# Kernel optimization log

Measured on AMD Instinct MI355X. Metric: run time of the kernel, lower is better.

## Reference

```python
import jax, jax.numpy as jnp
import numpy as np
from jax import lax

B, S, I, H, O, T = 8, 1024, 512, 1024, 512, 8
THRESH = 0.5


def setup_inputs() -> dict:
    key = jax.random.key(0)
    k = jax.random.split(key, 5)
    return {
        "x": jax.random.normal(k[0], (B, S, I), dtype=jnp.float32),
        "w1": jax.random.normal(k[1], (H, I), dtype=jnp.float32) * (1.0 / np.sqrt(I)),
        "b1": jax.random.normal(k[2], (H,), dtype=jnp.float32) * 0.01,
        "w2": jax.random.normal(k[3], (O, H), dtype=jnp.float32) * (1.0 / np.sqrt(H)),
        "b2": jax.random.normal(k[4], (O,), dtype=jnp.float32) * 0.01,
    }


def reference(x, w1, b1, w2, b2):
    # x: (B, S, I). Precompute the input current once (same every timestep).
    inp_cur = jnp.einsum("bsi,hi->bsh", x, w1) + b1  # (B, S, H)
    mem1_0 = jnp.zeros((B, S, H), dtype=x.dtype)
    mem2_0 = jnp.zeros((B, S, O), dtype=x.dtype)

    def step(carry, _):
        mem1, mem2 = carry
        mem1 = mem1 + inp_cur
        spike1 = (mem1 > THRESH).astype(x.dtype)
        mem1 = mem1 * (mem1 <= THRESH).astype(x.dtype)  # reset fired neurons
        mem2 = mem2 + jnp.einsum("bsh,oh->bso", spike1, w2) + b2
        spike2 = (mem2 > THRESH).astype(x.dtype)
        mem2 = mem2 * (mem2 <= THRESH).astype(x.dtype)
        return (mem1, mem2), spike2

    _, spikes = lax.scan(step, (mem1_0, mem2_0), None, length=T)  # (T, B, S, O)
    return jnp.moveaxis(spikes, 0, 1)  # stack on dim=1 -> (B, T, S, O)
```

## Files before the change

### kernel.cpp

```cpp
#include <hip/hip_runtime.h>

static constexpr int B_ = 8, S_ = 1024, I_ = 512, H_ = 1024, O_ = 512, T_ = 8;
static constexpr int M_ = B_ * S_;
static constexpr float TH = 0.5f;

__global__ __launch_bounds__(256) void k1(const float* __restrict__ X,
                                          const float* __restrict__ W1,
                                          const float* __restrict__ B1,
                                          unsigned char* __restrict__ SPB) {
  __shared__ float As[16][132];
  __shared__ float Bs[16][68];
  const int tid = threadIdx.x;
  const int tx = tid & 15, ty = tid >> 4;
  const int rowBase = blockIdx.x * 128, colBase = blockIdx.y * 64;

  float acc[8][4];
#pragma unroll
  for (int i = 0; i < 8; ++i)
#pragma unroll
    for (int j = 0; j < 4; ++j) acc[i][j] = 0.f;

  for (int it = 0; it < 32; ++it) {
#pragma unroll
    for (int l = 0; l < 2; ++l) {
      int f = tid + l * 256;
      int rr = f >> 2, kq = (f & 3) << 2;
      float4 va = *(const float4*)&X[(size_t)(rowBase + rr) * I_ + it * 16 + kq];
      As[kq + 0][rr] = va.x; As[kq + 1][rr] = va.y;
      As[kq + 2][rr] = va.z; As[kq + 3][rr] = va.w;
    }
    {
      int rr = tid >> 2, kq = (tid & 3) << 2;
      float4 vb = *(const float4*)&W1[(size_t)(colBase + rr) * I_ + it * 16 + kq];
      Bs[kq + 0][rr] = vb.x; Bs[kq + 1][rr] = vb.y;
      Bs[kq + 2][rr] = vb.z; Bs[kq + 3][rr] = vb.w;
    }
    __syncthreads();
#pragma unroll
    for (int k = 0; k < 16; ++k) {
      float a[8], b[4];
      *(float4*)&a[0] = *(const float4*)&As[k][ty * 8];
      *(float4*)&a[4] = *(const float4*)&As[k][ty * 8 + 4];
      *(float4*)&b[0] = *(const float4*)&Bs[k][tx * 4];
#pragma unroll
      for (int i = 0; i < 8; ++i)
#pragma unroll
        for (int j = 0; j < 4; ++j) acc[i][j] = fmaf(a[i], b[j], acc[i][j]);
    }
    __syncthreads();
  }

#pragma unroll
  for (int i = 0; i < 8; ++i) {
    int row = rowBase + ty * 8 + i;
    unsigned char by[4];
#pragma unroll
    for (int j = 0; j < 4; ++j) {
      int col = colBase + tx * 4 + j;
      float c = acc[i][j] + B1[col];
      float m = 0.f;
      unsigned bits = 0;
#pragma unroll
      for (int t = 0; t < 8; ++t) {
        m = m + c;
        bool s = m > TH;
        bits |= (s ? 1u : 0u) << t;
        m = s ? 0.f : m;
      }
      by[j] = (unsigned char)bits;
    }
    uchar4 pk; pk.x = by[0]; pk.y = by[1]; pk.z = by[2]; pk.w = by[3];
    *(uchar4*)&SPB[(size_t)row * H_ + colBase + tx * 4] = pk;
  }
}

__global__ __launch_bounds__(256) void k2(const unsigned char* __restrict__ SP,
                                          const float* __restrict__ W2,
                                          const float* __restrict__ B2,
                                          float* __restrict__ out, int t) {
  __shared__ float As0[16][68];
  __shared__ float As1[16][68];
  __shared__ float Bs0[16][68];
  __shared__ float Bs1[16][68];
  const int tid = threadIdx.x;
  const int tx = tid & 15, ty = tid >> 4;
  const int rowBase = blockIdx.x * 64, colBase = blockIdx.y * 64;

  float cur0[4][4], cur1[4][4];
#pragma unroll
  for (int i = 0; i < 4; ++i)
#pragma unroll
    for (int j = 0; j < 4; ++j) { cur0[i][j] = 0.f; cur1[i][j] = 0.f; }

  for (int it = 0; it < 32; ++it) {
    {
      int rr = tid >> 2, bq = (tid & 3) << 2;
      unsigned u0 = *(const unsigned*)&SP[(size_t)(rowBase + rr) * H_ + it * 16 + bq];
      As0[bq + 0][rr] = (float)((u0 >> t) & 1u);
      As0[bq + 1][rr] = (float)((u0 >> (8 + t)) & 1u);
      As0[bq + 2][rr] = (float)((u0 >> (16 + t)) & 1u);
      As0[bq + 3][rr] = (float)((u0 >> (24 + t)) & 1u);
      unsigned u1 = *(const unsigned*)&SP[(size_t)(rowBase + rr) * H_ + 512 + it * 16 + bq];
      As1[bq + 0][rr] = (float)((u1 >> t) & 1u);
      As1[bq + 1][rr] = (float)((u1 >> (8 + t)) & 1u);
      As1[bq + 2][rr] = (float)((u1 >> (16 + t)) & 1u);
      As1[bq + 3][rr] = (float)((u1 >> (24 + t)) & 1u);
      float4 vb0 = *(const float4*)&W2[(size_t)(colBase + rr) * H_ + it * 16 + bq];
      Bs0[bq + 0][rr] = vb0.x; Bs0[bq + 1][rr] = vb0.y;
      Bs0[bq + 2][rr] = vb0.z; Bs0[bq + 3][rr] = vb0.w;
      float4 vb1 = *(const float4*)&W2[(size_t)(colBase + rr) * H_ + 512 + it * 16 + bq];
      Bs1[bq + 0][rr] = vb1.x; Bs1[bq + 1][rr] = vb1.y;
      Bs1[bq + 2][rr] = vb1.z; Bs1[bq + 3][rr] = vb1.w;
    }
    __syncthreads();
#pragma unroll
    for (int k = 0; k < 16; ++k) {
      float a0[4], b0[4], a1[4], b1v[4];
      *(float4*)&a0[0] = *(const float4*)&As0[k][ty * 4];
      *(float4*)&b0[0] = *(const float4*)&Bs0[k][tx * 4];
      *(float4*)&a1[0] = *(const float4*)&As1[k][ty * 4];
      *(float4*)&b1v[0] = *(const float4*)&Bs1[k][tx * 4];
#pragma unroll
      for (int i = 0; i < 4; ++i)
#pragma unroll
        for (int j = 0; j < 4; ++j) {
          cur0[i][j] = fmaf(a0[i], b0[j], cur0[i][j]);
          cur1[i][j] = fmaf(a1[i], b1v[j], cur1[i][j]);
        }
    }
    __syncthreads();
  }

  const int col0 = colBase + tx * 4;
  float4 b2v = *(const float4*)&B2[col0];
#pragma unroll
  for (int i = 0; i < 4; ++i) {
    int row = rowBase + ty * 4 + i;
    int bb = row >> 10;
    int ss = row & (S_ - 1);
    size_t slot_t = (((size_t)bb * T_ + t) * S_ + ss) * O_ + col0;
    float4 mp;
    if (t == 0) mp = make_float4(0.f, 0.f, 0.f, 0.f);
    else mp = *(const float4*)&out[slot_t];
    float d[4], mm[4];
#pragma unroll
    for (int j = 0; j < 4; ++j)
      d[j] = cur0[i][j] + cur1[i][j];
    mm[0] = (mp.x + d[0]) + b2v.x;
    mm[1] = (mp.y + d[1]) + b2v.y;
    mm[2] = (mp.z + d[2]) + b2v.z;
    mm[3] = (mp.w + d[3]) + b2v.w;
    float4 sp, mn;
    sp.x = (mm[0] > TH) ? 1.f : 0.f;  mn.x = (mm[0] > TH) ? 0.f : mm[0];
    sp.y = (mm[1] > TH) ? 1.f : 0.f;  mn.y = (mm[1] > TH) ? 0.f : mm[1];
    sp.z = (mm[2] > TH) ? 1.f : 0.f;  mn.z = (mm[2] > TH) ? 0.f : mm[2];
    sp.w = (mm[3] > TH) ? 1.f : 0.f;  mn.w = (mm[3] > TH) ? 0.f : mm[3];
    *(float4*)&out[slot_t] = sp;
    if (t < T_ - 1) {
      size_t slot_n = (((size_t)bb * T_ + (t + 1)) * S_ + ss) * O_ + col0;
      *(float4*)&out[slot_n] = mn;
    }
  }
}

extern "C" void kernel_launch(void* const* d_in, const int* in_sizes, int n_in,
                              void* d_out, int out_size, void* d_ws, size_t ws_size,
                              hipStream_t stream) {
  const float* x  = (const float*)d_in[0];
  const float* w1 = (const float*)d_in[1];
  const float* b1 = (const float*)d_in[2];
  const float* w2 = (const float*)d_in[3];
  const float* b2 = (const float*)d_in[4];
  float* out = (float*)d_out;

  unsigned char* spikeB = (unsigned char*)d_ws;

  k1<<<dim3(M_ / 128, H_ / 64), 256, 0, stream>>>(x, w1, b1, spikeB);
  for (int t = 0; t < T_; ++t)
    k2<<<dim3(M_ / 64, O_ / 64), 256, 0, stream>>>(spikeB, w2, b2, out, t);
}
```

Measured before the change: 982.6 us.

## Prefetch next K tile into registers and double K tile depth in both GEMMs

Both GEMM kernels now load the next K-slice from global memory into registers while computing on the current shared-memory tile. The tile depth goes from 16 to 32, which halves the number of loop iterations and barrier pairs. This is meant to hide global-load latency behind the FMA loop and cut synchronisation overhead. It costs more registers and twice the shared memory per block, which may lower occupancy.

```diff
diff --git a/kernel.cpp b/kernel.cpp
--- a/kernel.cpp
+++ b/kernel.cpp
@@ -8,11 +8,12 @@
                                           const float* __restrict__ W1,
                                           const float* __restrict__ B1,
                                           unsigned char* __restrict__ SPB) {
-  __shared__ float As[16][132];
-  __shared__ float Bs[16][68];
+  __shared__ float As[32][132];
+  __shared__ float Bs[32][68];
   const int tid = threadIdx.x;
   const int tx = tid & 15, ty = tid >> 4;
   const int rowBase = blockIdx.x * 128, colBase = blockIdx.y * 64;
+  const int rr = tid >> 3, kq = (tid & 7) << 2;
 
   float acc[8][4];
 #pragma unroll
@@ -20,24 +21,35 @@
 #pragma unroll
     for (int j = 0; j < 4; ++j) acc[i][j] = 0.f;
 
-  for (int it = 0; it < 32; ++it) {
+  float4 pa[4], pb[2];
+#define K1_LOAD(IT)                                                            \
+  {                                                                            \
+    _Pragma("unroll")                                                          \
+    for (int l = 0; l < 4; ++l)                                                \
+      pa[l] = *(const float4*)&X[(size_t)(rowBase + rr + l * 32) * I_ +        \
+                                 (IT) * 32 + kq];                              \
+    _Pragma("unroll")                                                          \
+    for (int l = 0; l < 2; ++l)                                                \
+      pb[l] = *(const float4*)&W1[(size_t)(colBase + rr + l * 32) * I_ +       \
+                                  (IT) * 32 + kq];                             \
+  }
+
+  K1_LOAD(0);
+  for (int it = 0; it < 16; ++it) {
+#pragma unroll
+    for (int l = 0; l < 4; ++l) {
+      As[kq + 0][rr + l * 32] = pa[l].x; As[kq + 1][rr + l * 32] = pa[l].y;
+      As[kq + 2][rr + l * 32] = pa[l].z; As[kq + 3][rr + l * 32] = pa[l].w;
+    }
 #pragma unroll
     for (int l = 0; l < 2; ++l) {
-      int f = tid + l * 256;
-      int rr = f >> 2, kq = (f & 3) << 2;
-      float4 va = *(const float4*)&X[(size_t)(rowBase + rr) * I_ + it * 16 + kq];
-      As[kq + 0][rr] = va.x; As[kq + 1][rr] = va.y;
-      As[kq + 2][rr] = va.z; As[kq + 3][rr] = va.w;
-    }
-    {
-      int rr = tid >> 2, kq = (tid & 3) << 2;
-      float4 vb = *(const float4*)&W1[(size_t)(colBase + rr) * I_ + it * 16 + kq];
-      Bs[kq + 0][rr] = vb.x; Bs[kq + 1][rr] = vb.y;
-      Bs[kq + 2][rr] = vb.z; Bs[kq + 3][rr] = vb.w;
-    }
-    __syncthreads();
-#pragma unroll
-    for (int k = 0; k < 16; ++k) {
+      Bs[kq + 0][rr + l * 32] = pb[l].x; Bs[kq + 1][rr + l * 32] = pb[l].y;
+      Bs[kq + 2][rr + l * 32] = pb[l].z; Bs[kq + 3][rr + l * 32] = pb[l].w;
+    }
+    __syncthreads();
+    if (it + 1 < 16) K1_LOAD(it + 1);
+#pragma unroll
+    for (int k = 0; k < 32; ++k) {
       float a[8], b[4];
       *(float4*)&a[0] = *(const float4*)&As[k][ty * 8];
       *(float4*)&a[4] = *(const float4*)&As[k][ty * 8 + 4];
@@ -49,6 +61,7 @@
     }
     __syncthreads();
   }
+#undef K1_LOAD
 
 #pragma unroll
   for (int i = 0; i < 8; ++i) {
@@ -78,13 +91,14 @@
                                           const float* __restrict__ W2,
                                           const float* __restrict__ B2,
                                           float* __restrict__ out, int t) {
-  __shared__ float As0[16][68];
-  __shared__ float As1[16][68];
-  __shared__ float Bs0[16][68];
-  __shared__ float Bs1[16][68];
+  __shared__ float As0[32][68];
+  __shared__ float As1[32][68];
+  __shared__ float Bs0[32][68];
+  __shared__ float Bs1[32][68];
   const int tid = threadIdx.x;
   const int tx = tid & 15, ty = tid >> 4;
   const int rowBase = blockIdx.x * 64, colBase = blockIdx.y * 64;
+  const int rr = tid >> 3, bq = (tid & 7) << 2;
 
   float cur0[4][4], cur1[4][4];
 #pragma unroll
@@ -92,29 +106,40 @@
 #pragma unroll
     for (int j = 0; j < 4; ++j) { cur0[i][j] = 0.f; cur1[i][j] = 0.f; }
 
-  for (int it = 0; it < 32; ++it) {
-    {
-      int rr = tid >> 2, bq = (tid & 3) << 2;
-      unsigned u0 = *(const unsigned*)&SP[(size_t)(rowBase + rr) * H_ + it * 16 + bq];
-      As0[bq + 0][rr] = (float)((u0 >> t) & 1u);
-      As0[bq + 1][rr] = (float)((u0 >> (8 + t)) & 1u);
-      As0[bq + 2][rr] = (float)((u0 >> (16 + t)) & 1u);
-      As0[bq + 3][rr] = (float)((u0 >> (24 + t)) & 1u);
-      unsigned u1 = *(const unsigned*)&SP[(size_t)(rowBase + rr) * H_ + 512 + it * 16 + bq];
-      As1[bq + 0][rr] = (float)((u1 >> t) & 1u);
-      As1[bq + 1][rr] = (float)((u1 >> (8 + t)) & 1u);
-      As1[bq + 2][rr] = (float)((u1 >> (16 + t)) & 1u);
-      As1[bq + 3][rr] = (float)((u1 >> (24 + t)) & 1u);
-      float4 vb0 = *(const float4*)&W2[(size_t)(colBase + rr) * H_ + it * 16 + bq];
-      Bs0[bq + 0][rr] = vb0.x; Bs0[bq + 1][rr] = vb0.y;
-      Bs0[bq + 2][rr] = vb0.z; Bs0[bq + 3][rr] = vb0.w;
-      float4 vb1 = *(const float4*)&W2[(size_t)(colBase + rr) * H_ + 512 + it * 16 + bq];
-      Bs1[bq + 0][rr] = vb1.x; Bs1[bq + 1][rr] = vb1.y;
-      Bs1[bq + 2][rr] = vb1.z; Bs1[bq + 3][rr] = vb1.w;
-    }
-    __syncthreads();
-#pragma unroll
-    for (int k = 0; k < 16; ++k) {
+  unsigned pu0[2], pu1[2];
+  float4 pb0[2], pb1[2];
+#define K2_LOAD(IT)                                                            \
+  {                                                                            \
+    _Pragma("unroll")                                                          \
+    for (int l = 0; l < 2; ++l) {                                              \
+      const size_t rowOff = (size_t)(rowBase + rr + l * 32) * H_;              \
+      pu0[l] = *(const unsigned*)&SP[rowOff + (IT) * 32 + bq];                 \
+      pu1[l] = *(const unsigned*)&SP[rowOff + 512 + (IT) * 32 + bq];           \
+      const size_t colOff = (size_t)(colBase + rr + l * 32) * H_;              \
+      pb0[l] = *(const float4*)&W2[colOff + (IT) * 32 + bq];                   \
+      pb1[l] = *(const float4*)&W2[colOff + 512 + (IT) * 32 + bq];             \
+    }                                                                          \
+  }
+
+  K2_LOAD(0);
+  for (int it = 0; it < 16; ++it) {
+#pragma unroll
+    for (int l = 0; l < 2; ++l) {
+      const int rl = rr + l * 32;
+#pragma unroll
+      for (int c = 0; c < 4; ++c) {
+        As0[bq + c][rl] = (float)((pu0[l] >> (8 * c + t)) & 1u);
+        As1[bq + c][rl] = (float)((pu1[l] >> (8 * c + t)) & 1u);
+      }
+      Bs0[bq + 0][rl] = pb0[l].x; Bs0[bq + 1][rl] = pb0[l].y;
+      Bs0[bq + 2][rl] = pb0[l].z; Bs0[bq + 3][rl] = pb0[l].w;
+      Bs1[bq + 0][rl] = pb1[l].x; Bs1[bq + 1][rl] = pb1[l].y;
+      Bs1[bq + 2][rl] = pb1[l].z; Bs1[bq + 3][rl] = pb1[l].w;
+    }
+    __syncthreads();
+    if (it + 1 < 16) K2_LOAD(it + 1);
+#pragma unroll
+    for (int k = 0; k < 32; ++k) {
       float a0[4], b0[4], a1[4], b1v[4];
       *(float4*)&a0[0] = *(const float4*)&As0[k][ty * 4];
       *(float4*)&b0[0] = *(const float4*)&Bs0[k][tx * 4];
@@ -130,6 +155,7 @@
     }
     __syncthreads();
   }
+#undef K2_LOAD
 
   const int col0 = colBase + tx * 4;
   float4 b2v = *(const float4*)&B2[col0];
```

Measured after the change: 1.062 ms. 8.0% more time.
